# Optimization experiments

Measured on AMD Instinct MI355X. Metric: run time of the kernel, lower is better.

The kernel has to match this reference:

```python
import jax, jax.numpy as jnp
import numpy as np


def setup_inputs() -> dict:
    key = jax.random.key(0)
    k1, k2 = jax.random.split(key)
    B, C, H, W = 8, 21, 512, 512
    inp = jax.random.normal(k1, (B, C, H, W), dtype=jnp.float32)
    target = jax.random.randint(k2, (B, H, W), 0, C, dtype=jnp.int64)
    return {"input": inp, "target": target}


def reference(input, target):
    # input: (B, C, H, W) logits; target: (B, H, W) int labels in [0, C)
    B, C, H, W = input.shape
    N = H * W
    logits = input.reshape(B, C, N)                      # (B, C, N)
    tgt = target.reshape(B, N)                           # (B, N)
    tgt_f = tgt.astype(logits.dtype)

    probs = jax.nn.softmax(logits, axis=1)               # (B, C, N)
    # foreground mask per class: (B, C, N)
    fg = (tgt[:, None, :] == jnp.arange(C)[None, :, None]).astype(logits.dtype)
    errors = jnp.abs(fg - probs)                         # (B, C, N)

    # descending sort along N, vectorized over all (B, C) rows
    perm = jnp.argsort(-errors, axis=2)                  # (B, C, N)
    errors_sorted = jnp.take_along_axis(errors, perm, axis=2)
    # faithful to kornia: gather the raw float labels (not the binary mask)
    tgt_bc = jnp.broadcast_to(tgt_f[:, None, :], (B, C, N))
    target_sorted = jnp.take_along_axis(tgt_bc, perm, axis=2)  # (B, C, N)

    tsum = jnp.sum(target_sorted, axis=2, keepdims=True)       # (B, C, 1)
    intersection = tsum - jnp.cumsum(target_sorted, axis=2)
    union = tsum + jnp.cumsum(1.0 - target_sorted, axis=2)
    gradient = 1.0 - intersection / union                      # (B, C, N)
    # in-place diff along last axis: g[..., 1:] -= g[..., :-1]
    gradient = jnp.concatenate(
        [gradient[..., :1], gradient[..., 1:] - gradient[..., :-1]], axis=-1
    )

    # per-class loss = mean over batch of sum over pixels; final = mean over classes
    loss_bc = jnp.sum(jax.nn.relu(errors_sorted) * gradient, axis=2)  # (B, C)
    return jnp.mean(loss_bc)
```

## Files before the change

kernel.cpp:

```cpp
#include <hip/hip_runtime.h>


#define NB     8
#define NC     21
#define NPIX   262144
#define NROWS  (NB * NC)
#define NBINS  768
#define CHUNKS 32
#define CHUNK  (NPIX / CHUNKS)

__global__ __launch_bounds__(1024) void k_fused(
    const float* __restrict__ x,
    const int* __restrict__ tgt,
    unsigned* __restrict__ partial) {
  __shared__ unsigned hist[NC * NBINS];
  int tid = threadIdx.x;
  for (int i = tid; i < NC * NBINS; i += 1024) hist[i] = 0;
  __syncthreads();

  int b     = blockIdx.x >> 5;
  int chunk = blockIdx.x & 31;
  const float* xb = x + (size_t)b * NC * NPIX + (size_t)chunk * CHUNK;
  const int*   tb = tgt + (size_t)b * NPIX + (size_t)chunk * CHUNK;

  #pragma unroll
  for (int g = 0; g < 4; ++g) {
    int n2 = (g * 1024 + tid) * 2;

    float Z0 = 0.f, Z1 = 0.f;
    #pragma unroll
    for (int c = 0; c < NC; ++c) {
      float2 t = *(const float2*)(xb + (size_t)c * NPIX + n2);
      Z0 += __expf(t.x);
      Z1 += __expf(t.y);
    }
    float L0 = __logf(Z0);
    float L1 = __logf(Z1);

    int2 tv = *(const int2*)(tb + n2);

    #pragma unroll
    for (int c = 0; c < NC; ++c) {
      float2 t = *(const float2*)(xb + (size_t)c * NPIX + n2);
      unsigned* hr = hist + c * NBINS;

      float p0 = __expf(t.x - L0);
      float e0 = fabsf(((c == tv.x) ? 1.0f : 0.0f) - p0);
      unsigned fb0 = __float_as_uint(e0);
      int      fx0 = (int)(fb0 >> 23) - 127;
      unsigned k0;
      if (fx0 < -12) k0 = 0u;
      else {
        k0 = (((unsigned)(fx0 + 12)) << 6) | ((fb0 >> 17) & 63u);
        if (k0 > NBINS - 1) k0 = NBINS - 1;
      }
      atomicAdd(hr + k0, (1u << 18) | (unsigned)tv.x);

      float p1 = __expf(t.y - L1);
      float e1 = fabsf(((c == tv.y) ? 1.0f : 0.0f) - p1);
      unsigned fb1 = __float_as_uint(e1);
      int      fx1 = (int)(fb1 >> 23) - 127;
      unsigned k1;
      if (fx1 < -12) k1 = 0u;
      else {
        k1 = (((unsigned)(fx1 + 12)) << 6) | ((fb1 >> 17) & 63u);
        if (k1 > NBINS - 1) k1 = NBINS - 1;
      }
      atomicAdd(hr + k1, (1u << 18) | (unsigned)tv.y);
    }
  }
  __syncthreads();

  unsigned* op = partial + (size_t)blockIdx.x * NC * NBINS;
  for (int i = tid; i < NC * NBINS; i += 1024) op[i] = hist[i];
}

__device__ inline unsigned long long shfl_up_u64(unsigned long long v, int off) {
  unsigned lo = (unsigned)v, hi = (unsigned)(v >> 32);
  lo = (unsigned)__shfl_up((int)lo, off, 64);
  hi = (unsigned)__shfl_up((int)hi, off, 64);
  return ((unsigned long long)hi << 32) | lo;
}
__device__ inline unsigned long long shfl_down_u64(unsigned long long v, int off) {
  unsigned lo = (unsigned)v, hi = (unsigned)(v >> 32);
  lo = (unsigned)__shfl_down((int)lo, off, 64);
  hi = (unsigned)__shfl_down((int)hi, off, 64);
  return ((unsigned long long)hi << 32) | lo;
}

__global__ __launch_bounds__(768) void k_scan(
    const unsigned* __restrict__ partial,
    float* __restrict__ out) {
  int row  = blockIdx.x;
  int b    = row / NC;
  int c    = row - b * NC;
  int tid  = threadIdx.x;
  int lane = tid & 63;
  int wave = tid >> 6;

  __shared__ unsigned long long hist0[NBINS];
  __shared__ unsigned long long wtot[12];
  __shared__ double wred[12];
  __shared__ double sT;

  {
    const unsigned* pp = partial + ((size_t)(b * CHUNKS) * NC + c) * NBINS + tid;
    unsigned long long cnt = 0, ls = 0;
    #pragma unroll 8
    for (int j = 0; j < CHUNKS; ++j) {
      unsigned v = pp[(size_t)j * NC * NBINS];
      cnt += (v >> 18);
      ls  += (v & 0x3FFFFu);
    }
    hist0[tid] = (cnt << 32) | ls;
  }
  __syncthreads();

  unsigned long long tot = hist0[tid];
  #pragma unroll
  for (int off = 32; off > 0; off >>= 1) tot += shfl_down_u64(tot, off);
  if (lane == 0) wtot[wave] = tot;
  __syncthreads();
  if (tid == 0) {
    unsigned long long g = 0;
    #pragma unroll
    for (int w = 0; w < 12; ++w) g += wtot[w];
    sT = (double)(unsigned)(g & 0xffffffffULL);
  }
  __syncthreads();
  double T = sT;
  __syncthreads();

  int bin = (NBINS - 1) - tid;
  unsigned long long v = hist0[bin];

  unsigned long long s = v;
  #pragma unroll
  for (int off = 1; off < 64; off <<= 1) {
    unsigned long long u = shfl_up_u64(s, off);
    if (lane >= off) s += u;
  }
  if (lane == 63) wtot[wave] = s;
  __syncthreads();

  unsigned long long woff = 0;
  for (int w = 0; w < wave; ++w) woff += wtot[w];
  unsigned long long excl = s - v + woff;

  double acc = 0.0;
  unsigned n = (unsigned)(v >> 32);
  if (n) {
    unsigned sl = (unsigned)(v & 0xffffffffu);
    unsigned cb = (unsigned)(excl >> 32);
    unsigned sb = (unsigned)(excl & 0xffffffffu);
    double Sb = (double)sb + (double)sl;
    double gb = 1.0 - (T - Sb) / (T + (double)(cb + n) - Sb);
    double ga = (cb == 0) ? 0.0
                          : 1.0 - (T - (double)sb) / (T + (double)cb - (double)sb);
    unsigned key = (unsigned)bin;
    unsigned ex  = key >> 6, mant = key & 63u;
    float e = ldexpf(1.0f + ((float)mant + 0.5f) * 0.015625f, (int)ex - 12);
    acc = (double)e * (gb - ga);
  }

  #pragma unroll
  for (int off = 32; off > 0; off >>= 1) acc += __shfl_down(acc, off, 64);
  if (lane == 0) wred[wave] = acc;
  __syncthreads();
  if (tid == 0) {
    double ssum = 0.0;
    #pragma unroll
    for (int w = 0; w < 12; ++w) ssum += wred[w];
    atomicAdd(out, (float)(ssum * (1.0 / (double)NROWS)));
  }
}

extern "C" void kernel_launch(void* const* d_in, const int* in_sizes, int n_in,
                              void* d_out, int out_size, void* d_ws, size_t ws_size,
                              hipStream_t stream) {
  const float* x  = (const float*)d_in[0];
  const int* tgt  = (const int*)d_in[1];
  float* out      = (float*)d_out;
  unsigned* partial = (unsigned*)d_ws;

  hipMemsetAsync(d_out, 0, sizeof(float), stream);
  k_fused<<<NB * CHUNKS, 1024, 0, stream>>>(x, tgt, partial);
  k_scan<<<NROWS, NBINS, 0, stream>>>(partial, out);
}
```

Before: 287.3 us.

## Shrink LDS histogram to one class at a time and double chunk count

The fused kernel now keeps a single-class 768-bin histogram in shared memory instead of all 21 classes, and flushes it after each class with two barriers. Per-pixel log-sum-exp values are staged in shared memory. Each thread now handles 4 pixels with float4 loads, and the chunk count doubles to 64. The aim is to cut LDS use per block so more blocks fit per CU. The cost is 42 barriers per block, more partial histograms for the scan kernel to read, and heavier atomic contention on the smaller per-class histogram.

```diff
diff --git a/kernel.cpp b/kernel.cpp
--- a/kernel.cpp
+++ b/kernel.cpp
@@ -6,73 +6,70 @@
 #define NPIX   262144
 #define NROWS  (NB * NC)
 #define NBINS  768
-#define CHUNKS 32
+#define CHUNKS 64
 #define CHUNK  (NPIX / CHUNKS)
 
-__global__ __launch_bounds__(1024) void k_fused(
+__device__ __forceinline__ void bin_px(float xv, float Lq, unsigned lab, int c,
+                                       unsigned* hist) {
+  float p = __expf(xv - Lq);
+  float e = fabsf((((int)lab == c) ? 1.0f : 0.0f) - p);
+  unsigned fb = __float_as_uint(e);
+  int      fx = (int)(fb >> 23) - 127;
+  unsigned k;
+  if (fx < -12) k = 0u;
+  else {
+    k = (((unsigned)(fx + 12)) << 6) | ((fb >> 17) & 63u);
+    if (k > NBINS - 1) k = NBINS - 1;
+  }
+  atomicAdd(hist + k, (1u << 18) | lab);
+}
+
+__global__ __launch_bounds__(1024, 8) void k_fused(
     const float* __restrict__ x,
     const int* __restrict__ tgt,
     unsigned* __restrict__ partial) {
-  __shared__ unsigned hist[NC * NBINS];
+  __shared__ float    Ls[CHUNK];
+  __shared__ unsigned hist[NBINS];
   int tid = threadIdx.x;
-  for (int i = tid; i < NC * NBINS; i += 1024) hist[i] = 0;
-  __syncthreads();
+  for (int i = tid; i < NBINS; i += 1024) hist[i] = 0;
 
-  int b     = blockIdx.x >> 5;
-  int chunk = blockIdx.x & 31;
+  int b     = blockIdx.x >> 6;
+  int chunk = blockIdx.x & 63;
   const float* xb = x + (size_t)b * NC * NPIX + (size_t)chunk * CHUNK;
   const int*   tb = tgt + (size_t)b * NPIX + (size_t)chunk * CHUNK;
 
+  int n4 = tid * 4;
+
+  float Z0 = 0.f, Z1 = 0.f, Z2 = 0.f, Z3 = 0.f;
   #pragma unroll
-  for (int g = 0; g < 4; ++g) {
-    int n2 = (g * 1024 + tid) * 2;
+  for (int c = 0; c < NC; ++c) {
+    float4 t = *(const float4*)(xb + (size_t)c * NPIX + n4);
+    Z0 += __expf(t.x); Z1 += __expf(t.y); Z2 += __expf(t.z); Z3 += __expf(t.w);
+  }
+  float4 Lv;
+  Lv.x = __logf(Z0); Lv.y = __logf(Z1); Lv.z = __logf(Z2); Lv.w = __logf(Z3);
+  *(float4*)(Ls + n4) = Lv;
 
-    float Z0 = 0.f, Z1 = 0.f;
-    #pragma unroll
-    for (int c = 0; c < NC; ++c) {
-      float2 t = *(const float2*)(xb + (size_t)c * NPIX + n2);
-      Z0 += __expf(t.x);
-      Z1 += __expf(t.y);
-    }
-    float L0 = __logf(Z0);
-    float L1 = __logf(Z1);
-
-    int2 tv = *(const int2*)(tb + n2);
-
-    #pragma unroll
-    for (int c = 0; c < NC; ++c) {
-      float2 t = *(const float2*)(xb + (size_t)c * NPIX + n2);
-      unsigned* hr = hist + c * NBINS;
-
-      float p0 = __expf(t.x - L0);
-      float e0 = fabsf(((c == tv.x) ? 1.0f : 0.0f) - p0);
-      unsigned fb0 = __float_as_uint(e0);
-      int      fx0 = (int)(fb0 >> 23) - 127;
-      unsigned k0;
-      if (fx0 < -12) k0 = 0u;
-      else {
-        k0 = (((unsigned)(fx0 + 12)) << 6) | ((fb0 >> 17) & 63u);
-        if (k0 > NBINS - 1) k0 = NBINS - 1;
-      }
-      atomicAdd(hr + k0, (1u << 18) | (unsigned)tv.x);
-
-      float p1 = __expf(t.y - L1);
-      float e1 = fabsf(((c == tv.y) ? 1.0f : 0.0f) - p1);
-      unsigned fb1 = __float_as_uint(e1);
-      int      fx1 = (int)(fb1 >> 23) - 127;
-      unsigned k1;
-      if (fx1 < -12) k1 = 0u;
-      else {
-        k1 = (((unsigned)(fx1 + 12)) << 6) | ((fb1 >> 17) & 63u);
-        if (k1 > NBINS - 1) k1 = NBINS - 1;
-      }
-      atomicAdd(hr + k1, (1u << 18) | (unsigned)tv.y);
-    }
-  }
+  int4 tv = *(const int4*)(tb + n4);
+  unsigned tl = (unsigned)tv.x | ((unsigned)tv.y << 8) |
+                ((unsigned)tv.z << 16) | ((unsigned)tv.w << 24);
   __syncthreads();
 
   unsigned* op = partial + (size_t)blockIdx.x * NC * NBINS;
-  for (int i = tid; i < NC * NBINS; i += 1024) op[i] = hist[i];
+  for (int c = 0; c < NC; ++c) {
+    float4 t  = *(const float4*)(xb + (size_t)c * NPIX + n4);
+    float4 Lq = *(const float4*)(Ls + n4);
+    bin_px(t.x, Lq.x,  tl        & 255u, c, hist);
+    bin_px(t.y, Lq.y, (tl >>  8) & 255u, c, hist);
+    bin_px(t.z, Lq.z, (tl >> 16) & 255u, c, hist);
+    bin_px(t.w, Lq.w, (tl >> 24) & 255u, c, hist);
+    __syncthreads();
+    for (int i = tid; i < NBINS; i += 1024) {
+      op[(size_t)c * NBINS + i] = hist[i];
+      hist[i] = 0;
+    }
+    __syncthreads();
+  }
 }
 
 __device__ inline unsigned long long shfl_up_u64(unsigned long long v, int off) {
```

New measurement: 283.8 us. No clear change (-1.2%).
